# Performance work log

Hardware: AMD Instinct MI355X
Metric: run time of the kernel (lower is better)

The kernel has to match this reference:

```python
import jax, jax.numpy as jnp
import numpy as np

C_Q = 256
C_KV = 256
C_HID = 32
N_HEADS = 8
INF = 1e9


def setup_inputs() -> dict:
    key = jax.random.key(0)
    ks = jax.random.split(key, 9)
    B, Q, KV = 4, 2048, 2048
    d = N_HEADS * C_HID
    glorot_q = (6.0 / (C_Q + d)) ** 0.5
    glorot_kv = (6.0 / (C_KV + d)) ** 0.5
    return {
        "input_q": jax.random.normal(ks[0], (B, Q, C_Q), dtype=jnp.float32),
        "input_kv": jax.random.normal(ks[1], (B, KV, C_KV), dtype=jnp.float32),
        "mask": jax.random.randint(ks[2], (B, 1, 1, KV), 0, 2).astype(jnp.float32),
        "bias": jax.random.normal(ks[3], (1, N_HEADS, Q, KV), dtype=jnp.float32),
        "w_q": jax.random.uniform(ks[4], (C_Q, d), jnp.float32, -glorot_q, glorot_q),
        "w_k": jax.random.uniform(ks[5], (C_KV, d), jnp.float32, -glorot_kv, glorot_kv),
        "w_v": jax.random.uniform(ks[6], (C_KV, d), jnp.float32, -glorot_kv, glorot_kv),
        "w_o": jnp.zeros((d, C_Q), dtype=jnp.float32),  # 'final' init -> zeros
        "b_o": jnp.zeros((C_Q,), dtype=jnp.float32),
    }


def reference(input_q, input_kv, mask, bias, w_q, w_k, w_v, w_o, b_o):
    B, Q, _ = input_q.shape
    KV = input_kv.shape[1]
    # project and split heads: [B, H, L, c]
    q = (input_q @ w_q).reshape(B, Q, N_HEADS, C_HID).transpose(0, 2, 1, 3)
    k = (input_kv @ w_k).reshape(B, KV, N_HEADS, C_HID).transpose(0, 2, 1, 3)
    v = (input_kv @ w_v).reshape(B, KV, N_HEADS, C_HID).transpose(0, 2, 1, 3)
    q = q / jnp.sqrt(jnp.asarray(C_HID, q.dtype))
    # scores [B, H, Q, KV] with mask-bias and additive bias before softmax
    a = jnp.einsum("bhqc,bhkc->bhqk", q, k)
    a = a + (mask - 1.0) * INF
    if bias is not None:
        a = a + bias
    a = jax.nn.softmax(a, axis=-1)
    out = jnp.einsum("bhqk,bhkc->bhqc", a, v)  # [B, H, Q, c]
    out = out.transpose(0, 2, 1, 3).reshape(B, Q, N_HEADS * C_HID)
    return out @ w_o + b_o
```

## Files before the change

### kernel.cpp

```cpp
#include <hip/hip_runtime.h>
#include <hip/hip_bf16.h>
#include <math.h>

#define B    4
#define QL   2048
#define KVL  2048
#define CQ   256
#define CKV  256
#define CH   32
#define NH   8
#define DM   256
#define QB   128
#define KVB  128
#define NSTRIP (KVL / KVB)

typedef __attribute__((ext_vector_type(8)))  short short8;
typedef __attribute__((ext_vector_type(4)))  float f32x4;
typedef __attribute__((ext_vector_type(16))) float f32x16;
typedef __attribute__((ext_vector_type(4)))  unsigned int u32x4;

static __device__ __forceinline__ short f2bf(float x) {
    __hip_bfloat16 h = __float2bfloat16(x);
    return __builtin_bit_cast(short, h);
}
static __device__ __forceinline__ unsigned int pkbf(float lo, float hi) {
    return (unsigned int)(unsigned short)f2bf(lo) |
           ((unsigned int)(unsigned short)f2bf(hi) << 16);
}

__global__ __launch_bounds__(256) void prep_cvt(
    const float* __restrict__ src, short* __restrict__ dst, int n8)
{
    int i = blockIdx.x * 256 + threadIdx.x;
    if (i >= n8) return;
    const float4* s = (const float4*)src + (size_t)i * 2;
    float4 a = s[0], b = s[1];
    short8 o = { f2bf(a.x), f2bf(a.y), f2bf(a.z), f2bf(a.w),
                 f2bf(b.x), f2bf(b.y), f2bf(b.z), f2bf(b.w) };
    *((short8*)dst + i) = o;
}

__global__ __launch_bounds__(256) void prep_wT(
    const float* __restrict__ w, short* __restrict__ wt, int K, int N)
{
    __shared__ float tile[32][33];
    const int bx = blockIdx.x * 32;
    const int by = blockIdx.y * 32;
    const int tx = threadIdx.x & 31, ty = threadIdx.x >> 5;
    #pragma unroll
    for (int i = 0; i < 32; i += 8)
        tile[ty + i][tx] = w[(size_t)(by + ty + i) * N + bx + tx];
    __syncthreads();
    #pragma unroll
    for (int i = 0; i < 32; i += 8)
        wt[(size_t)(bx + ty + i) * K + by + tx] = f2bf(tile[tx][ty + i]);
}

__global__ __launch_bounds__(256) void gemm_mfma(
    const short* __restrict__ A, const short* __restrict__ BT,
    const float* __restrict__ bias, float* __restrict__ outf,
    short* __restrict__ outb,
    int M, int N, int K, float alpha, int mode)
{
    __shared__ __align__(16) short As[64][40];
    __shared__ __align__(16) short Bs[64][40];

    const int t   = threadIdx.x;
    const int m0  = blockIdx.y * 64, n0 = blockIdx.x * 64;
    const int lane = t & 63, w = t >> 6;
    const int c16 = lane & 15, g = lane >> 4;
    const int wm  = (w & 1) * 32, wn = (w >> 1) * 32;
    const int lr  = t >> 2, lc = (t & 3) * 8;

    f32x4 acc[2][2] = {};

    for (int k0 = 0; k0 < K; k0 += 32) {
        __syncthreads();
        *(short8*)&As[lr][lc] = *(const short8*)(A  + (size_t)(m0 + lr) * K + k0 + lc);
        *(short8*)&Bs[lr][lc] = *(const short8*)(BT + (size_t)(n0 + lr) * K + k0 + lc);
        __syncthreads();

        short8 af[2], bf[2];
        #pragma unroll
        for (int i = 0; i < 2; i++) {
            af[i] = *(const short8*)&As[wm + i * 16 + c16][g * 8];
            bf[i] = *(const short8*)&Bs[wn + i * 16 + c16][g * 8];
        }
        #pragma unroll
        for (int i = 0; i < 2; i++)
            #pragma unroll
            for (int j = 0; j < 2; j++)
                acc[i][j] = __builtin_amdgcn_mfma_f32_16x16x32_bf16(af[i], bf[j], acc[i][j], 0, 0, 0);
    }

    #pragma unroll
    for (int i = 0; i < 2; i++) {
        #pragma unroll
        for (int j = 0; j < 2; j++) {
            #pragma unroll
            for (int r = 0; r < 4; r++) {
                int m = m0 + wm + i * 16 + g * 4 + r;
                int n = n0 + wn + j * 16 + c16;
                float v = acc[i][j][r] * alpha;
                if (mode == 0) {
                    outf[(size_t)m * N + n] = v + (bias ? bias[n] : 0.0f);
                } else {
                    int bb = m >> 11, l = m & 2047;
                    int hh = n >> 5,  cc = n & 31;
                    if (mode == 1)
                        outb[(((size_t)bb * NH + hh) * QL + l) * CH + cc] = f2bf(v);
                    else
                        outb[(((size_t)bb * NH + hh) * CH + cc) * (size_t)KVL + l] = f2bf(v);
                }
            }
        }
    }
}

__global__ __launch_bounds__(512)
__attribute__((amdgpu_waves_per_eu(4, 4)))
void fattn(
    const short* __restrict__ qbf, const short* __restrict__ kbf,
    const short* __restrict__ vtb, const float* __restrict__ mask,
    const float* __restrict__ bias, short* __restrict__ aob)
{
    __shared__ __align__(16) short Kl[2][KVB * 32];
    __shared__ __align__(16) short Vl[2][32 * KVB];
    __shared__ __align__(16) float Ml[KVL];

    const int t    = threadIdx.x;
    const int w    = t >> 6;
    const int wq   = w & 3;
    const int ws   = w >> 2;
    const int lane = t & 63;
    const int l31  = lane & 31;
    const int hi   = lane >> 5;

    const int q0 = blockIdx.x * QB;
    const int h  = blockIdx.y, b = blockIdx.z;
    const int bh = b * NH + h;
    const int ws64 = ws * 64;

    constexpr float L2E  = 1.4426950408889634f;
    constexpr float MBIG = 1e9f * L2E;
    constexpr float MOFF = -(1e9f * L2E) - 40.0f * L2E;

    const short* qrow = qbf + ((size_t)bh * QL + q0 + wq * 32 + l31) * CH;
    short8 qf0 = *(const short8*)(qrow + hi * 8);
    short8 qf1 = *(const short8*)(qrow + 16 + hi * 8);

    {
        float4 mv = *(const float4*)(mask + (size_t)b * KVL + t * 4);
        float4 o0 = { fmaf(mv.x, MBIG, MOFF), fmaf(mv.y, MBIG, MOFF),
                      fmaf(mv.z, MBIG, MOFF), fmaf(mv.w, MBIG, MOFF) };
        *(float4*)&Ml[t * 4] = o0;
    }

    const int rowK = t >> 2, kch = t & 3;
    const short* ksrc = kbf + (size_t)bh * KVL * CH + (size_t)rowK * CH + kch * 8;
    const int kbyte = (rowK * 64 + kch * 16) ^ ((rowK & 7) << 4);
    const int rowV = t >> 4, segV = t & 15;
    const short* vsrc = vtb + (size_t)bh * CH * KVL + (size_t)rowV * KVL + segV * 8;
    const int vbyte = (rowV * 256 + segV * 16) ^ ((rowV & 7) << 4);

    short8 kr0 = *(const short8*)ksrc;
    short8 vr0 = *(const short8*)vsrc;

    const float* brow = bias + ((size_t)h * QL + q0 + wq * 32 + l31) * KVL;

    float4 biA[4], biB[4];
    #pragma unroll
    for (int rr = 0; rr < 4; ++rr)
        biA[rr] = *(const float4*)(brow + ws64 + rr * 8 + hi * 4);

    f32x16 O;
    #pragma unroll
    for (int r = 0; r < 16; ++r) O[r] = 0.0f;
    float lp0 = 0.f, lp1 = 0.f, lp2 = 0.f, lp3 = 0.f;

#define SUB_BODY(SO32, BC, BN, NEXTCOL, GUARD)                                 \
    {                                                                          \
        if (GUARD) {                                                           \
            _Pragma("unroll")                                                  \
            for (int rr = 0; rr < 4; ++rr)                                     \
                BN[rr] = *(const float4*)(brow + (NEXTCOL) + rr * 8 + hi * 4); \
        }                                                                      \
        f32x16 Cb;                                                             \
        _Pragma("unroll")                                                      \
        for (int rr = 0; rr < 4; ++rr) {                                       \
            float4 mt = *(const float4*)&Ml[kv0 + (SO32) + rr * 8 + hi * 4];   \
            Cb[4 * rr + 0] = fmaf(BC[rr].x, L2E, mt.x);                        \
            Cb[4 * rr + 1] = fmaf(BC[rr].y, L2E, mt.y);                        \
            Cb[4 * rr + 2] = fmaf(BC[rr].z, L2E, mt.z);                        \
            Cb[4 * rr + 3] = fmaf(BC[rr].w, L2E, mt.w);                        \
        }                                                                      \
        const int krow32 = (SO32) + l31;                                       \
        const int kswz   = (krow32 & 7) << 4;                                  \
        short8 ka0 = *(const short8*)(klb + ((krow32 * 64 + hi * 16) ^ kswz)); \
        short8 ka1 = *(const short8*)(klb + ((krow32 * 64 + 32 + hi * 16) ^ kswz)); \
        __builtin_amdgcn_s_setprio(1);                                         \
        f32x16 S = __builtin_amdgcn_mfma_f32_32x32x16_bf16(ka0, qf0, Cb, 0, 0, 0); \
        S = __builtin_amdgcn_mfma_f32_32x32x16_bf16(ka1, qf1, S, 0, 0, 0);     \
        __builtin_amdgcn_s_setprio(0);                                         \
        unsigned int a1, a2, b1, b2, c1, c2, d1, d2;                           \
        {   float e0 = __builtin_amdgcn_exp2f(S[0]);                           \
            float e1 = __builtin_amdgcn_exp2f(S[1]);                           \
            float e2 = __builtin_amdgcn_exp2f(S[2]);                           \
            float e3 = __builtin_amdgcn_exp2f(S[3]);                           \
            lp0 += e0 + e1;  lp1 += e2 + e3;                                   \
            a1 = pkbf(e0, e1);  a2 = pkbf(e2, e3);  }                          \
        {   float e0 = __builtin_amdgcn_exp2f(S[4]);                           \
            float e1 = __builtin_amdgcn_exp2f(S[5]);                           \
            float e2 = __builtin_amdgcn_exp2f(S[6]);                           \
            float e3 = __builtin_amdgcn_exp2f(S[7]);                           \
            lp0 += e0 + e1;  lp1 += e2 + e3;                                   \
            b1 = pkbf(e0, e1);  b2 = pkbf(e2, e3);  }                          \
        {   float e0 = __builtin_amdgcn_exp2f(S[8]);                           \
            float e1 = __builtin_amdgcn_exp2f(S[9]);                           \
            float e2 = __builtin_amdgcn_exp2f(S[10]);                          \
            float e3 = __builtin_amdgcn_exp2f(S[11]);                          \
            lp2 += e0 + e1;  lp3 += e2 + e3;                                   \
            c1 = pkbf(e0, e1);  c2 = pkbf(e2, e3);  }                          \
        {   float e0 = __builtin_amdgcn_exp2f(S[12]);                          \
            float e1 = __builtin_amdgcn_exp2f(S[13]);                          \
            float e2 = __builtin_amdgcn_exp2f(S[14]);                          \
            float e3 = __builtin_amdgcn_exp2f(S[15]);                          \
            lp2 += e0 + e1;  lp3 += e2 + e3;                                   \
            d1 = pkbf(e0, e1);  d2 = pkbf(e2, e3);  }                          \
        asm("v_permlane32_swap_b32 %0, %1" : "+v"(a1), "+v"(b1));              \
        asm("v_permlane32_swap_b32 %0, %1" : "+v"(a2), "+v"(b2));              \
        asm("v_permlane32_swap_b32 %0, %1" : "+v"(c1), "+v"(d1));              \
        asm("v_permlane32_swap_b32 %0, %1" : "+v"(c2), "+v"(d2));              \
        u32x4 f0v = { a1, a2, b1, b2 };                                        \
        u32x4 f1v = { c1, c2, d1, d2 };                                        \
        short8 pf0 = __builtin_bit_cast(short8, f0v);                          \
        short8 pf1 = __builtin_bit_cast(short8, f1v);                          \
        const int vswz = (l31 & 7) << 4;                                       \
        short8 vf0 = *(const short8*)(vlb + ((l31 * 256 + (SO32) * 2 + hi * 16) ^ vswz)); \
        short8 vf1 = *(const short8*)(vlb + ((l31 * 256 + (SO32) * 2 + 32 + hi * 16) ^ vswz)); \
        __builtin_amdgcn_s_setprio(1);                                         \
        O = __builtin_amdgcn_mfma_f32_32x32x16_bf16(pf0, vf0, O, 0, 0, 0);     \
        O = __builtin_amdgcn_mfma_f32_32x32x16_bf16(pf1, vf1, O, 0, 0, 0);     \
        __builtin_amdgcn_s_setprio(0);                                         \
    }

    #pragma unroll 1
    for (int it = 0; it < NSTRIP; ++it) {
        const int kv0 = it * KVB;
        char* klb = (char*)Kl[it & 1];
        char* vlb = (char*)Vl[it & 1];

        *(short8*)(klb + kbyte) = kr0;
        *(short8*)(vlb + vbyte) = vr0;
        __syncthreads();

        if (it + 1 < NSTRIP) {
            kr0 = *(const short8*)(ksrc + (size_t)(it + 1) * KVB * CH);
            vr0 = *(const short8*)(vsrc + (it + 1) * KVB);
        }

        SUB_BODY(ws64,      biA, biB, kv0 + ws64 + 32,  1);
        SUB_BODY(ws64 + 32, biB, biA, kv0 + KVB + ws64, (it + 1 < NSTRIP));
    }
#undef SUB_BODY

    float lpq = (lp0 + lp1) + (lp2 + lp3);
    lpq += __shfl_xor(lpq, 32);

    float* Ob = (float*)&Kl[0][0];
    float* Lb = (float*)&Vl[0][0];
    __syncthreads();
    if (ws == 1) {
        float* op = Ob + wq * 32 * 32;
        #pragma unroll
        for (int r = 0; r < 16; ++r) {
            int q = (r & 3) + 8 * (r >> 2) + 4 * hi;
            op[q * 32 + l31] = O[r];
        }
        if (lane < 32) Lb[wq * 32 + l31] = lpq;
    }
    __syncthreads();
    if (ws == 0) {
        const float* op = Ob + wq * 32 * 32;
        float ltot = lpq + Lb[wq * 32 + l31];
        float linv = 1.0f / ltot;
        short* aop = aob + ((size_t)b * QL + q0 + wq * 32) * DM + h * CH;
        #pragma unroll
        for (int r = 0; r < 16; ++r) {
            int q = (r & 3) + 8 * (r >> 2) + 4 * hi;
            float ov = O[r] + op[q * 32 + l31];
            float inv = __shfl(linv, q);
            aop[(size_t)q * DM + l31] = f2bf(ov * inv);
        }
    }
}

extern "C" void kernel_launch(void* const* d_in, const int* in_sizes, int n_in,
                              void* d_out, int out_size, void* d_ws, size_t ws_size,
                              hipStream_t stream)
{
    const float* input_q  = (const float*)d_in[0];
    const float* input_kv = (const float*)d_in[1];
    const float* mask     = (const float*)d_in[2];
    const float* bias     = (const float*)d_in[3];
    const float* w_q      = (const float*)d_in[4];
    const float* w_k      = (const float*)d_in[5];
    const float* w_v      = (const float*)d_in[6];
    const float* w_o      = (const float*)d_in[7];
    const float* b_o      = (const float*)d_in[8];
    float* out = (float*)d_out;

    const size_t TOK  = (size_t)B * QL;
    const size_t HEAD = (size_t)B * NH * QL * CH;

    short* qbf = (short*)d_ws;
    short* kbf = qbf + HEAD;
    short* vtb = kbf + HEAD;
    short* aob = vtb + HEAD;
    short* qx  = aob + HEAD;
    short* kvx = qx  + HEAD;
    short* wqT = kvx + HEAD;
    short* wkT = wqT + CQ * DM;
    short* wvT = wkT + CKV * DM;
    short* woT = wvT + CKV * DM;

    dim3 blk(256);
    const float qscale = 0.17677669529663687f * 1.4426950408889634f;

    prep_cvt<<<dim3((TOK * CQ / 8 + 255) / 256), blk, 0, stream>>>(input_q,  qx,  (int)(TOK * CQ / 8));
    prep_cvt<<<dim3((TOK * CKV / 8 + 255) / 256), blk, 0, stream>>>(input_kv, kvx, (int)(TOK * CKV / 8));
    prep_wT<<<dim3(DM / 32, CQ / 32),  blk, 0, stream>>>(w_q, wqT, CQ,  DM);
    prep_wT<<<dim3(DM / 32, CKV / 32), blk, 0, stream>>>(w_k, wkT, CKV, DM);
    prep_wT<<<dim3(DM / 32, CKV / 32), blk, 0, stream>>>(w_v, wvT, CKV, DM);
    prep_wT<<<dim3(CQ / 32, DM / 32),  blk, 0, stream>>>(w_o, woT, DM,  CQ);

    dim3 pgrid(DM / 64, TOK / 64);
    gemm_mfma<<<pgrid, blk, 0, stream>>>(qx,  wqT, nullptr, nullptr, qbf,
                                         (int)TOK, DM, CQ,  qscale, 1);
    gemm_mfma<<<pgrid, blk, 0, stream>>>(kvx, wkT, nullptr, nullptr, kbf,
                                         (int)TOK, DM, CKV, 1.0f, 1);
    gemm_mfma<<<pgrid, blk, 0, stream>>>(kvx, wvT, nullptr, nullptr, vtb,
                                         (int)TOK, DM, CKV, 1.0f, 2);

    fattn<<<dim3(QL / QB, NH, B), dim3(512), 0, stream>>>(
        qbf, kbf, vtb, mask, bias, aob);

    gemm_mfma<<<dim3(CQ / 64, TOK / 64), blk, 0, stream>>>(aob, woT, b_o, out, nullptr,
                                         (int)TOK, CQ, DM, 1.0f, 0);
}
```

Before: 125.0 us.

## Share bias tile across batches by assigning batch elements to waves

The attention kernel now gives each block 32 query rows of one head across all four batch elements, with the four wave groups handling different batches. The bias tile, which is batch-independent, is loaded by those waves for the same rows rather than by separate blocks per batch, so cache reuse of the large bias tensor should improve. The mask is stored in LDS as bf16 per batch, the KV strip shrinks to 64 with per-batch K/V LDS buffers, and the waves_per_eu attribute is dropped. The risks are more LDS per block, more blocks with fewer query rows each, and small rounding of the mask constants to bf16.

```diff
diff --git a/kernel.cpp b/kernel.cpp
--- a/kernel.cpp
+++ b/kernel.cpp
@@ -10,11 +10,11 @@
 #define CH   32
 #define NH   8
 #define DM   256
-#define QB   128
-#define KVB  128
+#define KVB  64
 #define NSTRIP (KVL / KVB)
 
 typedef __attribute__((ext_vector_type(8)))  short short8;
+typedef __attribute__((ext_vector_type(4)))  short short4v;
 typedef __attribute__((ext_vector_type(4)))  float f32x4;
 typedef __attribute__((ext_vector_type(16))) float f32x16;
 typedef __attribute__((ext_vector_type(4)))  unsigned int u32x4;
@@ -22,6 +22,10 @@
 static __device__ __forceinline__ short f2bf(float x) {
     __hip_bfloat16 h = __float2bfloat16(x);
     return __builtin_bit_cast(short, h);
+}
+static __device__ __forceinline__ float bf2f(short s) {
+    unsigned int u = ((unsigned int)(unsigned short)s) << 16;
+    return __builtin_bit_cast(float, u);
 }
 static __device__ __forceinline__ unsigned int pkbf(float lo, float hi) {
     return (unsigned int)(unsigned short)f2bf(lo) |
@@ -117,84 +121,112 @@
     }
 }
 
-__global__ __launch_bounds__(512)
-__attribute__((amdgpu_waves_per_eu(4, 4)))
-void fattn(
+__global__ __launch_bounds__(512) void fattn(
     const short* __restrict__ qbf, const short* __restrict__ kbf,
     const short* __restrict__ vtb, const float* __restrict__ mask,
     const float* __restrict__ bias, short* __restrict__ aob)
 {
-    __shared__ __align__(16) short Kl[2][KVB * 32];
-    __shared__ __align__(16) short Vl[2][32 * KVB];
-    __shared__ __align__(16) float Ml[KVL];
+    __shared__ __align__(16) short Kl[2][B][KVB * 32];
+    __shared__ __align__(16) short Vl[2][B][32 * KVB];
+    __shared__ __align__(16) short Mt[B][KVL];
 
     const int t    = threadIdx.x;
-    const int w    = t >> 6;
-    const int wq   = w & 3;
-    const int ws   = w >> 2;
+    const int wv   = t >> 6;
+    const int bq   = wv & 3;
+    const int ws   = wv >> 2;
     const int lane = t & 63;
     const int l31  = lane & 31;
     const int hi   = lane >> 5;
 
-    const int q0 = blockIdx.x * QB;
-    const int h  = blockIdx.y, b = blockIdx.z;
-    const int bh = b * NH + h;
-    const int ws64 = ws * 64;
+    const int q0 = blockIdx.x * 32;
+    const int h  = blockIdx.y;
+    const int bh = bq * NH + h;
+    const int ws32 = ws * 32;
 
     constexpr float L2E  = 1.4426950408889634f;
     constexpr float MBIG = 1e9f * L2E;
     constexpr float MOFF = -(1e9f * L2E) - 40.0f * L2E;
 
-    const short* qrow = qbf + ((size_t)bh * QL + q0 + wq * 32 + l31) * CH;
+    const short* qrow = qbf + ((size_t)bh * QL + q0 + l31) * CH;
     short8 qf0 = *(const short8*)(qrow + hi * 8);
     short8 qf1 = *(const short8*)(qrow + 16 + hi * 8);
 
     {
-        float4 mv = *(const float4*)(mask + (size_t)b * KVL + t * 4);
-        float4 o0 = { fmaf(mv.x, MBIG, MOFF), fmaf(mv.y, MBIG, MOFF),
-                      fmaf(mv.z, MBIG, MOFF), fmaf(mv.w, MBIG, MOFF) };
-        *(float4*)&Ml[t * 4] = o0;
-    }
-
-    const int rowK = t >> 2, kch = t & 3;
-    const short* ksrc = kbf + (size_t)bh * KVL * CH + (size_t)rowK * CH + kch * 8;
-    const int kbyte = (rowK * 64 + kch * 16) ^ ((rowK & 7) << 4);
-    const int rowV = t >> 4, segV = t & 15;
-    const short* vsrc = vtb + (size_t)bh * CH * KVL + (size_t)rowV * KVL + segV * 8;
-    const int vbyte = (rowV * 256 + segV * 16) ^ ((rowV & 7) << 4);
+        const int bm = t >> 7, idx = t & 127;
+        const float* mp = mask + (size_t)bm * KVL + idx * 16;
+        float4 m0 = *(const float4*)(mp);
+        float4 m1 = *(const float4*)(mp + 4);
+        float4 m2 = *(const float4*)(mp + 8);
+        float4 m3 = *(const float4*)(mp + 12);
+        short8 s0 = { f2bf(fmaf(m0.x, MBIG, MOFF)), f2bf(fmaf(m0.y, MBIG, MOFF)),
+                      f2bf(fmaf(m0.z, MBIG, MOFF)), f2bf(fmaf(m0.w, MBIG, MOFF)),
+                      f2bf(fmaf(m1.x, MBIG, MOFF)), f2bf(fmaf(m1.y, MBIG, MOFF)),
+                      f2bf(fmaf(m1.z, MBIG, MOFF)), f2bf(fmaf(m1.w, MBIG, MOFF)) };
+        short8 s1 = { f2bf(fmaf(m2.x, MBIG, MOFF)), f2bf(fmaf(m2.y, MBIG, MOFF)),
+                      f2bf(fmaf(m2.z, MBIG, MOFF)), f2bf(fmaf(m2.w, MBIG, MOFF)),
+                      f2bf(fmaf(m3.x, MBIG, MOFF)), f2bf(fmaf(m3.y, MBIG, MOFF)),
+                      f2bf(fmaf(m3.z, MBIG, MOFF)), f2bf(fmaf(m3.w, MBIG, MOFF)) };
+        *(short8*)&Mt[bm][idx * 16]     = s0;
+        *(short8*)&Mt[bm][idx * 16 + 8] = s1;
+    }
+
+    const int bk   = t >> 7, ik = t & 127;
+    const int krow = ik >> 1, khalf = ik & 1;
+    const short* ksrc = kbf + ((size_t)(bk * NH + h) * KVL + krow) * CH + khalf * 16;
+    const int kb0 = (krow * 64 + khalf * 32)      ^ ((krow & 7) << 4);
+    const int kb1 = (krow * 64 + khalf * 32 + 16) ^ ((krow & 7) << 4);
+    const int vrow = ik >> 2, vseg = ik & 3;
+    const short* vsrc = vtb + ((size_t)(bk * NH + h) * CH + vrow) * KVL + vseg * 16;
+    const int vb0 = (vrow * 128 + vseg * 32)      ^ ((vrow & 7) << 4);
+    const int vb1 = (vrow * 128 + vseg * 32 + 16) ^ ((vrow & 7) << 4);
 
     short8 kr0 = *(const short8*)ksrc;
+    short8 kr1 = *(const short8*)(ksrc + 8);
     short8 vr0 = *(const short8*)vsrc;
-
-    const float* brow = bias + ((size_t)h * QL + q0 + wq * 32 + l31) * KVL;
+    short8 vr1 = *(const short8*)(vsrc + 8);
+
+    const float* brow = bias + ((size_t)h * QL + q0 + l31) * KVL;
 
     float4 biA[4], biB[4];
     #pragma unroll
     for (int rr = 0; rr < 4; ++rr)
-        biA[rr] = *(const float4*)(brow + ws64 + rr * 8 + hi * 4);
+        biA[rr] = *(const float4*)(brow + ws32 + rr * 8 + hi * 4);
+
+    const short* mtb = &Mt[bq][0];
 
     f32x16 O;
     #pragma unroll
     for (int r = 0; r < 16; ++r) O[r] = 0.0f;
     float lp0 = 0.f, lp1 = 0.f, lp2 = 0.f, lp3 = 0.f;
 
-#define SUB_BODY(SO32, BC, BN, NEXTCOL, GUARD)                                 \
+#define STRIP_BODY(IT, BUF, BC, BN)                                            \
     {                                                                          \
-        if (GUARD) {                                                           \
+        char* kst = (char*)&Kl[BUF][bk][0];                                    \
+        char* vst = (char*)&Vl[BUF][bk][0];                                    \
+        *(short8*)(kst + kb0) = kr0;  *(short8*)(kst + kb1) = kr1;             \
+        *(short8*)(vst + vb0) = vr0;  *(short8*)(vst + vb1) = vr1;             \
+        __syncthreads();                                                       \
+        if ((IT) + 1 < NSTRIP) {                                               \
+            const short* kn = ksrc + (size_t)((IT) + 1) * KVB * CH;            \
+            const short* vn = vsrc + ((IT) + 1) * KVB;                         \
+            kr0 = *(const short8*)kn;  kr1 = *(const short8*)(kn + 8);         \
+            vr0 = *(const short8*)vn;  vr1 = *(const short8*)(vn + 8);         \
             _Pragma("unroll")                                                  \
             for (int rr = 0; rr < 4; ++rr)                                     \
-                BN[rr] = *(const float4*)(brow + (NEXTCOL) + rr * 8 + hi * 4); \
+                BN[rr] = *(const float4*)(brow + ((IT) + 1) * KVB + ws32 + rr * 8 + hi * 4); \
         }                                                                      \
+        const char* klb = (const char*)&Kl[BUF][bq][0];                        \
+        const char* vlb = (const char*)&Vl[BUF][bq][0];                        \
         f32x16 Cb;                                                             \
         _Pragma("unroll")                                                      \
         for (int rr = 0; rr < 4; ++rr) {                                       \
-            float4 mt = *(const float4*)&Ml[kv0 + (SO32) + rr * 8 + hi * 4];   \
-            Cb[4 * rr + 0] = fmaf(BC[rr].x, L2E, mt.x);                        \
-            Cb[4 * rr + 1] = fmaf(BC[rr].y, L2E, mt.y);                        \
-            Cb[4 * rr + 2] = fmaf(BC[rr].z, L2E, mt.z);                        \
-            Cb[4 * rr + 3] = fmaf(BC[rr].w, L2E, mt.w);                        \
+            short4v mt4 = *(const short4v*)(mtb + (IT) * KVB + ws32 + rr * 8 + hi * 4); \
+            Cb[4 * rr + 0] = fmaf(BC[rr].x, L2E, bf2f(mt4[0]));                \
+            Cb[4 * rr + 1] = fmaf(BC[rr].y, L2E, bf2f(mt4[1]));                \
+            Cb[4 * rr + 2] = fmaf(BC[rr].z, L2E, bf2f(mt4[2]));                \
+            Cb[4 * rr + 3] = fmaf(BC[rr].w, L2E, bf2f(mt4[3]));                \
         }                                                                      \
-        const int krow32 = (SO32) + l31;                                       \
+        const int krow32 = ws32 + l31;                                         \
         const int kswz   = (krow32 & 7) << 4;                                  \
         short8 ka0 = *(const short8*)(klb + ((krow32 * 64 + hi * 16) ^ kswz)); \
         short8 ka1 = *(const short8*)(klb + ((krow32 * 64 + 32 + hi * 16) ^ kswz)); \
@@ -236,8 +268,8 @@
         short8 pf0 = __builtin_bit_cast(short8, f0v);                          \
         short8 pf1 = __builtin_bit_cast(short8, f1v);                          \
         const int vswz = (l31 & 7) << 4;                                       \
-        short8 vf0 = *(const short8*)(vlb + ((l31 * 256 + (SO32) * 2 + hi * 16) ^ vswz)); \
-        short8 vf1 = *(const short8*)(vlb + ((l31 * 256 + (SO32) * 2 + 32 + hi * 16) ^ vswz)); \
+        short8 vf0 = *(const short8*)(vlb + ((l31 * 128 + ws * 64 + hi * 16) ^ vswz)); \
+        short8 vf1 = *(const short8*)(vlb + ((l31 * 128 + ws * 64 + 32 + hi * 16) ^ vswz)); \
         __builtin_amdgcn_s_setprio(1);                                         \
         O = __builtin_amdgcn_mfma_f32_32x32x16_bf16(pf0, vf0, O, 0, 0, 0);     \
         O = __builtin_amdgcn_mfma_f32_32x32x16_bf16(pf1, vf1, O, 0, 0, 0);     \
@@ -245,46 +277,33 @@
     }
 
     #pragma unroll 1
-    for (int it = 0; it < NSTRIP; ++it) {
-        const int kv0 = it * KVB;
-        char* klb = (char*)Kl[it & 1];
-        char* vlb = (char*)Vl[it & 1];
-
-        *(short8*)(klb + kbyte) = kr0;
-        *(short8*)(vlb + vbyte) = vr0;
-        __syncthreads();
-
-        if (it + 1 < NSTRIP) {
-            kr0 = *(const short8*)(ksrc + (size_t)(it + 1) * KVB * CH);
-            vr0 = *(const short8*)(vsrc + (it + 1) * KVB);
-        }
-
-        SUB_BODY(ws64,      biA, biB, kv0 + ws64 + 32,  1);
-        SUB_BODY(ws64 + 32, biB, biA, kv0 + KVB + ws64, (it + 1 < NSTRIP));
-    }
-#undef SUB_BODY
+    for (int pp = 0; pp < NSTRIP / 2; ++pp) {
+        STRIP_BODY(2 * pp,     0, biA, biB);
+        STRIP_BODY(2 * pp + 1, 1, biB, biA);
+    }
+#undef STRIP_BODY
 
     float lpq = (lp0 + lp1) + (lp2 + lp3);
     lpq += __shfl_xor(lpq, 32);
 
-    float* Ob = (float*)&Kl[0][0];
-    float* Lb = (float*)&Vl[0][0];
+    float* Ob = (float*)&Kl[0][0][0];
+    float* Lb = (float*)&Vl[0][0][0];
     __syncthreads();
     if (ws == 1) {
-        float* op = Ob + wq * 32 * 32;
+        float* op = Ob + bq * 32 * 32;
         #pragma unroll
         for (int r = 0; r < 16; ++r) {
             int q = (r & 3) + 8 * (r >> 2) + 4 * hi;
             op[q * 32 + l31] = O[r];
         }
-        if (lane < 32) Lb[wq * 32 + l31] = lpq;
+        if (lane < 32) Lb[bq * 32 + l31] = lpq;
     }
     __syncthreads();
     if (ws == 0) {
-        const float* op = Ob + wq * 32 * 32;
-        float ltot = lpq + Lb[wq * 32 + l31];
+        const float* op = Ob + bq * 32 * 32;
+        float ltot = lpq + Lb[bq * 32 + l31];
         float linv = 1.0f / ltot;
-        short* aop = aob + ((size_t)b * QL + q0 + wq * 32) * DM + h * CH;
+        short* aop = aob + ((size_t)bq * QL + q0) * DM + h * CH;
         #pragma unroll
         for (int r = 0; r < 16; ++r) {
             int q = (r & 3) + 8 * (r >> 2) + 4 * hi;
@@ -342,7 +361,7 @@
     gemm_mfma<<<pgrid, blk, 0, stream>>>(kvx, wvT, nullptr, nullptr, vtb,
                                          (int)TOK, DM, CKV, 1.0f, 2);
 
-    fattn<<<dim3(QL / QB, NH, B), dim3(512), 0, stream>>>(
+    fattn<<<dim3(QL / 32, NH), dim3(512), 0, stream>>>(
         qbf, kbf, vtb, mask, bias, aob);
 
     gemm_mfma<<<dim3(CQ / 64, TOK / 64), blk, 0, stream>>>(aob, woT, b_o, out, nullptr,
```

Measured after the change: 154.4 us. 1.24x slower.
